# Performance work log

Measured on AMD Instinct MI355X. Metric: run time of the kernel, lower is better.

## Reference

```python
import jax, jax.numpy as jnp
import numpy as np

N = 65536   # number of GP locations
M = 64      # max ancestor set size (contiguous window A(i) = {i-M+1..i})
B = 16384   # minibatch size


def setup_inputs() -> dict:
    rng = np.random.default_rng(0)
    i = np.arange(N)
    # CSR row lengths: U (lower-tri) row i has cols {max(0,i-M+1)..i}; V (upper-tri) row j has cols {j..min(j+M-1,N-1)}
    row_len_u = np.minimum(i + 1, M)
    row_len_v = np.minimum(M, N - i)
    crow_u = np.concatenate([[0], np.cumsum(row_len_u)]).astype(np.int32)
    crow_v = np.concatenate([[0], np.cumsum(row_len_v)]).astype(np.int32)
    nnz = int(crow_u[-1])  # 4192288, same for both matrices
    # off-diagonals small, diagonals near 1 (kept positive for logDet and solve stability)
    U_values = (rng.standard_normal(nnz) * 0.1).astype(np.float32)
    U_values[crow_u[1:] - 1] = rng.uniform(0.8, 1.2, N).astype(np.float32)  # last entry of row i = (i,i)
    V_values = (rng.standard_normal(nnz) * 0.1).astype(np.float32)
    V_values[crow_v[:-1]] = rng.uniform(0.8, 1.2, N).astype(np.float32)    # first entry of row i = (i,i)
    mean = (rng.standard_normal(N) * 0.5).astype(np.float32)
    mean_post = (rng.standard_normal(N) * 0.5).astype(np.float32)
    y = rng.standard_normal(N).astype(np.float32)
    mini_indices = rng.integers(0, N, B).astype(np.int32)
    return {
        'U_values': jnp.asarray(U_values),
        'V_values': jnp.asarray(V_values),
        'mean': jnp.asarray(mean),
        'mean_post': jnp.asarray(mean_post),
        'y': jnp.asarray(y),
        'noise': jnp.float32(0.1),
        'mini_indices': jnp.asarray(mini_indices),
        'crow_u': jnp.asarray(crow_u),
        'crow_v': jnp.asarray(crow_v),
    }


def reference(U_values, V_values, mean, mean_post, y, noise, mini_indices, crow_u, crow_v):
    nnz = U_values.shape[0]
    g = mini_indices                       # [B] selected rows
    L = jnp.minimum(g + 1, M)              # n_anc per selected row
    p = jnp.arange(M)
    valid = p[None, :] >= (M - L)[:, None]                 # [B,M] right-aligned validity mask
    anc = g[:, None] - (M - 1 - p)[None, :]                # global ancestor index at padded slot p
    anc_c = jnp.clip(anc, 0, N - 1)

    # get_sub_rows(UTrans): row g entries at A(g), right-aligned into [B,M]
    u_idx = crow_u[g][:, None] + (p[None, :] - (M - L)[:, None])
    U_sub = jnp.where(valid, U_values[jnp.clip(u_idx, 0, nnz - 1)], 0.0)

    # ragged mean difference gather (masked scatter in the original)
    md = jnp.where(valid, (mean - mean_post)[anc_c], 0.0)  # [B,M]

    # get_sub_mat(V, unit_diag=True): V[A(g),A(g)] bottom-right aligned, identity padding
    jrow = anc_c[:, :, None]                               # global row index of block row r
    icol = anc_c[:, None, :]                               # global col index of block col c
    vidx = crow_v[jrow] + (icol - jrow)                    # CSR value index of V[jrow, icol]
    blk_mask = (valid[:, :, None] & valid[:, None, :]
                & (p[None, :, None] <= p[None, None, :]))  # upper-tri of active block
    eye = jnp.eye(M, dtype=U_values.dtype)
    V_sub = jnp.where(blk_mask, V_values[jnp.clip(vidx, 0, nnz - 1)], eye[None, :, :])  # [B,M,M]

    # batched triangular solves
    ej = jnp.zeros((B, M), U_values.dtype).at[:, -1].set(1.0)
    sol_e = jax.scipy.linalg.solve_triangular(V_sub, ej[:, :, None], lower=False)
    marginalVarPost = jnp.sum(sol_e * sol_e, axis=(1, 2))  # [B]
    sol_u = jax.scipy.linalg.solve_triangular(V_sub, U_sub[:, :, None], lower=False)
    innerCov = -0.5 * jnp.sum(sol_u * sol_u)

    innerMean = -0.5 * jnp.sum(jnp.sum(U_sub * md, axis=1) ** 2)

    # log-determinant terms from diagonal gathers
    logDet = (jnp.sum(jnp.log(U_values[crow_u[g + 1] - 1]))
              - jnp.sum(jnp.log(V_values[crow_v[g]])))

    # Gaussian expected likelihood (noise is not None branch)
    resid = y[g] - mean_post[g]
    ell = (-0.5 * B * jnp.log(2.0 * jnp.pi * noise)
           - (jnp.sum(resid * resid) + jnp.sum(marginalVarPost)) / (2.0 * noise))

    return logDet + innerMean + innerCov + ell
```

## Files before the change

### kernel.cpp

```cpp
#include <hip/hip_runtime.h>
#include <math.h>

constexpr int kN = 65536;
constexpr int kB = 16384;
constexpr int kWaves = 4;
constexpr int kTileW = 3072;

static __device__ __forceinline__ float bcastf(float v, int lane) {
    union { float f; int i; } u;
    u.f = v;
    u.i = __builtin_amdgcn_readlane(u.i, lane);
    return u.f;
}

static __device__ __forceinline__ void gload_lds16(const float* g, float* l) {
    __builtin_amdgcn_global_load_lds(
        (const __attribute__((address_space(1))) void*)g,
        (__attribute__((address_space(3))) void*)l, 16, 0, 0);
}
static __device__ __forceinline__ void gload_lds4(const float* g, float* l) {
    __builtin_amdgcn_global_load_lds(
        (const __attribute__((address_space(1))) void*)g,
        (__attribute__((address_space(3))) void*)l, 4, 0, 0);
}

__global__ __launch_bounds__(64 * kWaves) void gp_solve_kernel(
    const float* __restrict__ Uv,
    const float* __restrict__ Vv,
    const float* __restrict__ mean,
    const float* __restrict__ mean_post,
    const float* __restrict__ y,
    const int*   __restrict__ gidx,
    const int*   __restrict__ crow_u,
    const int*   __restrict__ crow_v,
    const float* __restrict__ noise,
    float*       __restrict__ partial)
{
    __shared__ __align__(16) float lds[kWaves][kTileW];
    __shared__ float cred[kWaves];

    const int lane = (int)threadIdx.x & 63;
    const int wid  = (int)threadIdx.x >> 6;
    const int b    = (int)blockIdx.x * kWaves + wid;
    const int g    = gidx[b];
    float* myl = &lds[wid][0];

    const int  anc = g - 63 + lane;
    const bool vl  = (anc >= 0);
    const bool hot = (g >= 63) && (g <= kN - 64);

    const int L  = (g + 1 < 64) ? (g + 1) : 64;
    const int ub = (g >= 63) ? (2016 + 64 * (g - 63)) : crow_u[g];

    float uval = 0.0f, md = 0.0f;
    if (vl) {
        uval = Uv[ub + lane - (64 - L)];
        md   = mean[anc] - mean_post[anc];
    }
    const float yg  = y[g];
    const float mpg = mean_post[g];

    if (hot) {
        const float* srcA = Vv + 64 * (g - 63) + 4 * lane;
        #pragma unroll
        for (int k = 0; k < 8; ++k)
            gload_lds16(srcA + 256 * k, myl + 256 * k);
        const int rowoff = 64 * (lane >> 3) + 4 * (lane & 7);
        const float* srcB = Vv + 64 * (g - 31) + rowoff;
        #pragma unroll
        for (int k = 0; k < 4; ++k)
            gload_lds16(srcB + 512 * k, myl + 2048 + 256 * k);
    } else {
        int rowbase = 0;
        if (vl) rowbase = crow_v[anc];
        for (int j = 0; j < 64; ++j) {
            const int rbj = __builtin_amdgcn_readlane(rowbase, j);
            const int dst = (j < 32) ? 64 * j : (1024 + 32 * j);
            if (lane < 64 - j) {
                if (g - 63 + j >= 0)
                    gload_lds4(Vv + rbj + lane, myl + dst);
                else
                    myl[dst + lane] = 0.0f;
            }
        }
    }
    __syncthreads();

    const int rowstart = (lane < 32) ? (64 * lane) : (1024 + 32 * lane);
    const float d0 = myl[rowstart];
    const float diag = vl ? d0 : 1.0f;
    const float invd = 1.0f / diag;

    const float* vrowm = myl + (rowstart - lane);
    float v[64];
    #pragma unroll
    for (int i = 0; i < 64; ++i) v[i] = vrowm[i];

    float r_e = (lane == 63) ? 1.0f : 0.0f;
    float r_u = uval;
    float acc_e = 0.0f, acc_u = 0.0f;

    #pragma unroll
    for (int i = 63; i >= 0; --i) {
        const float t_e = r_e * invd;
        const float t_u = r_u * invd;
        const float s_e = bcastf(t_e, i);
        const float s_u = bcastf(t_u, i);
        r_e = fmaf(-v[i], s_e, r_e);
        r_u = fmaf(-v[i], s_u, r_u);
        acc_e = fmaf(s_e, s_e, acc_e);
        acc_u = fmaf(s_u, s_u, acc_u);
    }

    float dot = uval * md;
    #pragma unroll
    for (int m = 1; m < 64; m <<= 1)
        dot += __shfl_xor(dot, m, 64);

    const float ulast  = bcastf(uval, 63);
    const float vfirst = bcastf(diag, 63);

    if (lane == 0) {
        const float resid = yg - mpg;
        const float inv2n = 0.5f / noise[0];
        cred[wid] = logf(ulast) - logf(vfirst)
                  - 0.5f * dot * dot
                  - 0.5f * acc_u
                  - (resid * resid + acc_e) * inv2n;
    }
    __syncthreads();
    if (threadIdx.x == 0)
        partial[blockIdx.x] = (cred[0] + cred[1]) + (cred[2] + cred[3]);
}

__global__ __launch_bounds__(1024) void gp_reduce_kernel(
    const float* __restrict__ partial,
    const float* __restrict__ noise,
    float*       __restrict__ out)
{
    __shared__ float ws[16];
    const int t = (int)threadIdx.x;
    const float4 p = reinterpret_cast<const float4*>(partial)[t];
    float a = (p.x + p.y) + (p.z + p.w);
    #pragma unroll
    for (int m = 1; m < 64; m <<= 1)
        a += __shfl_xor(a, m, 64);
    if ((t & 63) == 0) ws[t >> 6] = a;
    __syncthreads();
    if (t == 0) {
        float tot = 0.0f;
        #pragma unroll
        for (int k = 0; k < 16; ++k) tot += ws[k];
        tot += -0.5f * (float)kB * logf(2.0f * 3.14159265358979323846f * noise[0]);
        out[0] = tot;
    }
}

extern "C" void kernel_launch(void* const* d_in, const int* in_sizes, int n_in,
                              void* d_out, int out_size, void* d_ws, size_t ws_size,
                              hipStream_t stream)
{
    const float* Uv        = (const float*)d_in[0];
    const float* Vv        = (const float*)d_in[1];
    const float* mean      = (const float*)d_in[2];
    const float* mean_post = (const float*)d_in[3];
    const float* y         = (const float*)d_in[4];
    const float* noise     = (const float*)d_in[5];
    const int*   gidx      = (const int*)d_in[6];
    const int*   crow_u    = (const int*)d_in[7];
    const int*   crow_v    = (const int*)d_in[8];
    float* partial = (float*)d_ws;

    gp_solve_kernel<<<dim3(kB / kWaves), dim3(64 * kWaves), 0, stream>>>(
        Uv, Vv, mean, mean_post, y, gidx, crow_u, crow_v, noise, partial);
    gp_reduce_kernel<<<dim3(1), dim3(1024), 0, stream>>>(
        partial, noise, (float*)d_out);
}
```

Measured before the change: 43.60 us.

## Use single-wave blocks with tighter banded LDS tile layout

The solve kernel switches from four waves per block to one wave per block. This removes the cross-wave __syncthreads and LDS partial reduction, and each wave writes its own partial; the reduce kernel now sums four times as many partials. The V tile is packed more tightly in LDS using 16-row groups whose widths shrink by 16 (2560 floats instead of 3072), with matching global-to-LDS load patterns. This is meant to cut LDS footprint and barrier cost to raise occupancy, at the cost of more blocks and more complex address arithmetic.

```diff
diff --git a/kernel.cpp b/kernel.cpp
--- a/kernel.cpp
+++ b/kernel.cpp
@@ -3,8 +3,7 @@
 
 constexpr int kN = 65536;
 constexpr int kB = 16384;
-constexpr int kWaves = 4;
-constexpr int kTileW = 3072;
+constexpr int kTileW = 2560;
 
 static __device__ __forceinline__ float bcastf(float v, int lane) {
     union { float f; int i; } u;
@@ -24,7 +23,12 @@
         (__attribute__((address_space(3))) void*)l, 4, 0, 0);
 }
 
-__global__ __launch_bounds__(64 * kWaves) void gp_solve_kernel(
+static __device__ __forceinline__ int row_start(int j) {
+    const int t = j >> 4;
+    return 1024 * t - 128 * t * (t - 1) + (64 - 16 * t) * (j - 16 * t);
+}
+
+__global__ __launch_bounds__(64) void gp_solve_kernel(
     const float* __restrict__ Uv,
     const float* __restrict__ Vv,
     const float* __restrict__ mean,
@@ -36,18 +40,15 @@
     const float* __restrict__ noise,
     float*       __restrict__ partial)
 {
-    __shared__ __align__(16) float lds[kWaves][kTileW];
-    __shared__ float cred[kWaves];
+    __shared__ __align__(16) float myl[kTileW];
 
-    const int lane = (int)threadIdx.x & 63;
-    const int wid  = (int)threadIdx.x >> 6;
-    const int b    = (int)blockIdx.x * kWaves + wid;
+    const int lane = (int)threadIdx.x;
+    const int b    = (int)blockIdx.x;
     const int g    = gidx[b];
-    float* myl = &lds[wid][0];
 
     const int  anc = g - 63 + lane;
     const bool vl  = (anc >= 0);
-    const bool hot = (g >= 63) && (g <= kN - 64);
+    const bool hot = (g >= 63) && (g <= kN - 63);
 
     const int L  = (g + 1 < 64) ? (g + 1) : 64;
     const int ub = (g >= 63) ? (2016 + 64 * (g - 63)) : crow_u[g];
@@ -61,40 +62,54 @@
     const float mpg = mean_post[g];
 
     if (hot) {
-        const float* srcA = Vv + 64 * (g - 63) + 4 * lane;
+        const float* base = Vv + 64 * (g - 63);
+        {
+            const float* src = base + 4 * lane;
+            #pragma unroll
+            for (int k = 0; k < 4; ++k)
+                gload_lds16(src + 256 * k, myl + 256 * k);
+        }
         #pragma unroll
-        for (int k = 0; k < 8; ++k)
-            gload_lds16(srcA + 256 * k, myl + 256 * k);
-        const int rowoff = 64 * (lane >> 3) + 4 * (lane & 7);
-        const float* srcB = Vv + 64 * (g - 31) + rowoff;
+        for (int k = 0; k < 3; ++k) {
+            const int w   = 256 * k + 4 * lane;
+            const int jj  = ((w >> 4) * 171) >> 9;
+            const int col = w - 48 * jj;
+            gload_lds16(base + 64 * (16 + jj) + col, myl + 1024 + 256 * k);
+        }
         #pragma unroll
-        for (int k = 0; k < 4; ++k)
-            gload_lds16(srcB + 512 * k, myl + 2048 + 256 * k);
+        for (int k = 0; k < 2; ++k) {
+            const int w = 256 * k + 4 * lane;
+            gload_lds16(base + 64 * (32 + (w >> 5)) + (w & 31), myl + 1792 + 256 * k);
+        }
+        {
+            const int w = 4 * lane;
+            gload_lds16(base + 64 * (48 + (w >> 4)) + (w & 15), myl + 2304);
+        }
     } else {
         int rowbase = 0;
         if (vl) rowbase = crow_v[anc];
         for (int j = 0; j < 64; ++j) {
-            const int rbj = __builtin_amdgcn_readlane(rowbase, j);
-            const int dst = (j < 32) ? 64 * j : (1024 + 32 * j);
+            union { float f; int i; } rb; rb.i = __builtin_amdgcn_readlane(rowbase, j);
+            const int dst = row_start(j);
             if (lane < 64 - j) {
                 if (g - 63 + j >= 0)
-                    gload_lds4(Vv + rbj + lane, myl + dst);
+                    gload_lds4(Vv + rb.i + lane, myl + dst);
                 else
                     myl[dst + lane] = 0.0f;
             }
         }
     }
-    __syncthreads();
+    asm volatile("s_waitcnt vmcnt(0) lgkmcnt(0)" ::: "memory");
 
-    const int rowstart = (lane < 32) ? (64 * lane) : (1024 + 32 * lane);
-    const float d0 = myl[rowstart];
+    const int rs = row_start(lane);
+    const float d0   = myl[rs];
     const float diag = vl ? d0 : 1.0f;
     const float invd = 1.0f / diag;
 
-    const float* vrowm = myl + (rowstart - lane);
+    const float* vrow = myl + (rs - lane);
     float v[64];
     #pragma unroll
-    for (int i = 0; i < 64; ++i) v[i] = vrowm[i];
+    for (int i = 0; i < 64; ++i) v[i] = vrow[i];
 
     float r_e = (lane == 63) ? 1.0f : 0.0f;
     float r_u = uval;
@@ -123,14 +138,11 @@
     if (lane == 0) {
         const float resid = yg - mpg;
         const float inv2n = 0.5f / noise[0];
-        cred[wid] = logf(ulast) - logf(vfirst)
-                  - 0.5f * dot * dot
-                  - 0.5f * acc_u
-                  - (resid * resid + acc_e) * inv2n;
+        partial[b] = logf(ulast) - logf(vfirst)
+                   - 0.5f * dot * dot
+                   - 0.5f * acc_u
+                   - (resid * resid + acc_e) * inv2n;
     }
-    __syncthreads();
-    if (threadIdx.x == 0)
-        partial[blockIdx.x] = (cred[0] + cred[1]) + (cred[2] + cred[3]);
 }
 
 __global__ __launch_bounds__(1024) void gp_reduce_kernel(
@@ -140,8 +152,12 @@
 {
     __shared__ float ws[16];
     const int t = (int)threadIdx.x;
-    const float4 p = reinterpret_cast<const float4*>(partial)[t];
-    float a = (p.x + p.y) + (p.z + p.w);
+    float a = 0.0f;
+    #pragma unroll
+    for (int k = 0; k < 4; ++k) {
+        const float4 p = reinterpret_cast<const float4*>(partial)[t + 1024 * k];
+        a += (p.x + p.y) + (p.z + p.w);
+    }
     #pragma unroll
     for (int m = 1; m < 64; m <<= 1)
         a += __shfl_xor(a, m, 64);
@@ -171,7 +187,7 @@
     const int*   crow_v    = (const int*)d_in[8];
     float* partial = (float*)d_ws;
 
-    gp_solve_kernel<<<dim3(kB / kWaves), dim3(64 * kWaves), 0, stream>>>(
+    gp_solve_kernel<<<dim3(kB), dim3(64), 0, stream>>>(
         Uv, Vv, mean, mean_post, y, gidx, crow_u, crow_v, noise, partial);
     gp_reduce_kernel<<<dim3(1), dim3(1024), 0, stream>>>(
         partial, noise, (float*)d_out);
```

Result: faster. 38.63 us (-11.4%).
